# Optimization experiments

Hardware: AMD Instinct MI355X
Metric: run time of the kernel (lower is better)

## Reference

```python
import jax, jax.numpy as jnp
import numpy as np

B, NC, F, V, D = 16384, 13, 26, 100000, 16
H1, H2 = 400, 400
DNN_IN = NC + F * D  # 13 + 416 = 429


def setup_inputs() -> dict:
    key = jax.random.key(0)
    ks = jax.random.split(key, 12)
    s = 0.02
    return {
        "continuous": jax.random.normal(ks[0], (B, NC), jnp.float32),
        "cat_idx": jax.random.randint(ks[1], (B, F), 0, V),
        "W_cont": jax.random.normal(ks[2], (NC, 1), jnp.float32) * s,
        "b_cont": jnp.zeros((1,), jnp.float32),
        "emb_first": jax.random.normal(ks[3], (F, V), jnp.float32) * s,
        "emb": jax.random.normal(ks[4], (F, V, D), jnp.float32) * s,
        "W1": jax.random.normal(ks[5], (DNN_IN, H1), jnp.float32) * s,
        "b1": jnp.zeros((H1,), jnp.float32),
        "W2": jax.random.normal(ks[6], (H1, H2), jnp.float32) * s,
        "b2": jnp.zeros((H2,), jnp.float32),
        "W_out": jax.random.normal(ks[7], (H2 + 1, 1), jnp.float32) * s,
        "b_out": jnp.zeros((1,), jnp.float32),
    }


def reference(continuous, cat_idx, W_cont, b_cont, emb_first, emb, W1, b1, W2, b2, W_out, b_out):
    f_ids = jnp.arange(F)  # column ids
    # FM first-order: continuous linear + per-column 1-dim embedding gather, summed over columns
    fm1_cat = emb_first[f_ids[None, :], cat_idx]          # [B, F]
    fm1 = continuous @ W_cont + b_cont + jnp.sum(fm1_cat, axis=1, keepdims=True)  # [B, 1]
    # FM second-order: per-column D-dim embedding gather
    E = emb[f_ids[None, :], cat_idx]                      # [B, F, D]
    sum_emb = jnp.sum(E, axis=1)                          # [B, D]
    fm2 = 0.5 * jnp.sum(sum_emb * sum_emb - jnp.sum(E * E, axis=1), axis=1, keepdims=True)  # [B, 1]
    fm_out = fm1 + fm2
    # DNN on [continuous | flattened embeddings]; Dropout(0.0) is identity
    dnn_in = jnp.concatenate([continuous, E.reshape(E.shape[0], -1)], axis=1)  # [B, 429]
    h = jax.nn.relu(dnn_in @ W1 + b1)
    h = jax.nn.relu(h @ W2 + b2)
    fusion = jnp.concatenate([fm_out, h], axis=1)         # [B, H2+1]
    return fusion @ W_out + b_out                          # [B, 1]
```

## Files before the change

kernel.cpp:

```cpp
#include <hip/hip_runtime.h>
#include <hip/hip_bf16.h>
#include <stdint.h>

#define NB    16384
#define NCONT 13
#define NF    26
#define NV    100000
#define ND    16
#define NH    400
#define K1    448
#define KP1   456
#define K2    416
#define KP2   424
#define ROWS  64

typedef __attribute__((ext_vector_type(8))) __bf16 bf16x8;
typedef __attribute__((ext_vector_type(8))) short short8;
typedef __attribute__((ext_vector_type(4))) float f32x4;

__device__ __forceinline__ short f2bf(float x) {
  union { float f; uint32_t u; } c; c.f = x;
  uint32_t r = (c.u + 0x7FFFu + ((c.u >> 16) & 1u)) >> 16;
  return (short)(uint16_t)r;
}

__global__ __launch_bounds__(256)
void prep_k(const float* __restrict__ W1, const float* __restrict__ W2,
            short* __restrict__ W1T, short* __restrict__ W2T) {
  int t = blockIdx.x * 256 + threadIdx.x;
  if (t < NH * K1) {
    int n = t / K1, k = t - n * K1;
    float v = 0.f;
    if (k < 416)       v = W1[(size_t)(13 + k) * NH + n];
    else if (k < 429)  v = W1[(size_t)(k - 416) * NH + n];
    W1T[t] = f2bf(v);
  } else {
    int u = t - NH * K1;
    int n = u / K2, k = u - n * K2;
    float v = (k < NH) ? W2[(size_t)k * NH + n] : 0.f;
    W2T[u] = f2bf(v);
  }
}

template <int K, int KP>
__device__ __forceinline__ void layer(const short* __restrict__ WT, const short* lds,
                                      int wave, bool w0, int lrow, int kq,
                                      f32x4 acc[4][7]) {
  const short* wb = WT + (size_t)(wave * 16 + lrow) * K + kq;
  bf16x8 wf[2][7], af[2][4];
#pragma unroll
  for (int j = 0; j < 7; j++)
    if (j < 6 || w0) wf[0][j] = *(const bf16x8*)(wb + (size_t)j * 64 * K);
#pragma unroll
  for (int i = 0; i < 4; i++)
    af[0][i] = *(const bf16x8*)(lds + (i * 16 + lrow) * KP + kq);
#pragma unroll
  for (int ks = 0; ks < K / 32; ks++) {
    const int cur = ks & 1, nxt = cur ^ 1;
    if (ks + 1 < K / 32) {
#pragma unroll
      for (int j = 0; j < 7; j++)
        if (j < 6 || w0)
          wf[nxt][j] = *(const bf16x8*)(wb + (size_t)j * 64 * K + (ks + 1) * 32);
#pragma unroll
      for (int i = 0; i < 4; i++)
        af[nxt][i] = *(const bf16x8*)(lds + (i * 16 + lrow) * KP + (ks + 1) * 32 + kq);
    }
#pragma unroll
    for (int i = 0; i < 4; i++)
#pragma unroll
      for (int j = 0; j < 7; j++)
        if (j < 6 || w0)
          acc[i][j] = __builtin_amdgcn_mfma_f32_16x16x32_bf16(af[cur][i], wf[cur][j], acc[i][j], 0, 0, 0);
  }
}

__global__ __launch_bounds__(256, 1)
void fused_k(const float* __restrict__ cont, const int* __restrict__ cat,
             const float* __restrict__ Wc, const float* __restrict__ bc,
             const float* __restrict__ emb1, const float* __restrict__ emb,
             const short* __restrict__ W1T, const float* __restrict__ b1,
             const short* __restrict__ W2T, const float* __restrict__ b2,
             const float* __restrict__ Wout, const float* __restrict__ bout,
             float* __restrict__ out) {
  __shared__ short buf[ROWS * KP1];
  __shared__ float lP[4][ROWS];
  __shared__ float lFM[ROWS];
  short* lA = buf;
  short* lH = buf;
  const int tid = threadIdx.x;
  const int bm = blockIdx.x * ROWS;

  {
    const int q  = tid & 3;
    const int rl = tid >> 2;
    const int b  = bm + rl;
    float se[16];
#pragma unroll
    for (int d = 0; d < 16; d++) se[d] = 0.f;
    float sumsq = 0.f, fm1 = 0.f;
    short* drow = lA + rl * KP1;

#pragma unroll
    for (int fi = 0; fi < 7; fi++) {
      const int f = q + 4 * fi;
      if (f < NF) {
        int idx = cat[(size_t)b * NF + f];
        const float4* ep = (const float4*)(emb + ((size_t)f * NV + idx) * ND);
        float4 e0 = ep[0], e1 = ep[1], e2 = ep[2], e3 = ep[3];
        fm1 += emb1[(size_t)f * NV + idx];
        se[0] += e0.x; se[1] += e0.y; se[2] += e0.z; se[3] += e0.w;
        se[4] += e1.x; se[5] += e1.y; se[6] += e1.z; se[7] += e1.w;
        se[8] += e2.x; se[9] += e2.y; se[10] += e2.z; se[11] += e2.w;
        se[12] += e3.x; se[13] += e3.y; se[14] += e3.z; se[15] += e3.w;
        sumsq += e0.x*e0.x + e0.y*e0.y + e0.z*e0.z + e0.w*e0.w
               + e1.x*e1.x + e1.y*e1.y + e1.z*e1.z + e1.w*e1.w
               + e2.x*e2.x + e2.y*e2.y + e2.z*e2.z + e2.w*e2.w
               + e3.x*e3.x + e3.y*e3.y + e3.z*e3.z + e3.w*e3.w;
        short8 p0, p1;
        p0[0]=f2bf(e0.x); p0[1]=f2bf(e0.y); p0[2]=f2bf(e0.z); p0[3]=f2bf(e0.w);
        p0[4]=f2bf(e1.x); p0[5]=f2bf(e1.y); p0[6]=f2bf(e1.z); p0[7]=f2bf(e1.w);
        p1[0]=f2bf(e2.x); p1[1]=f2bf(e2.y); p1[2]=f2bf(e2.z); p1[3]=f2bf(e2.w);
        p1[4]=f2bf(e3.x); p1[5]=f2bf(e3.y); p1[6]=f2bf(e3.z); p1[7]=f2bf(e3.w);
        *(short8*)(drow + f * 16)     = p0;
        *(short8*)(drow + f * 16 + 8) = p1;
      }
    }
#pragma unroll
    for (int d = 0; d < 16; d++) {
      se[d] += __shfl_xor(se[d], 1, 64);
      se[d] += __shfl_xor(se[d], 2, 64);
    }
    sumsq += __shfl_xor(sumsq, 1, 64);
    sumsq += __shfl_xor(sumsq, 2, 64);
    fm1   += __shfl_xor(fm1, 1, 64);
    fm1   += __shfl_xor(fm1, 2, 64);

    if (q == 0) {
      float s2 = 0.f;
#pragma unroll
      for (int d = 0; d < 16; d++) s2 += se[d] * se[d];
      float fm2 = 0.5f * (s2 - sumsq);
      float fmc = bc[0];
      short tail[32];
#pragma unroll
      for (int i = 0; i < NCONT; i++) {
        float c = cont[(size_t)b * NCONT + i];
        fmc += c * Wc[i];
        tail[i] = f2bf(c);
      }
#pragma unroll
      for (int i = NCONT; i < 32; i++) tail[i] = 0;
#pragma unroll
      for (int v = 0; v < 4; v++) {
        short8 tv;
#pragma unroll
        for (int e = 0; e < 8; e++) tv[e] = tail[v * 8 + e];
        *(short8*)(drow + 416 + v * 8) = tv;
      }
      lFM[rl] = fm1 + fmc + fm2;
    }
  }
  __syncthreads();

  const int lane = tid & 63;
  const int wave = tid >> 6;
  const int lrow = lane & 15;
  const int quad = lane >> 4;
  const int kq   = quad * 8;
  const bool w0  = (wave == 0);
  f32x4 acc[4][7];

#pragma unroll
  for (int i = 0; i < 4; i++)
#pragma unroll
    for (int j = 0; j < 7; j++)
#pragma unroll
      for (int r = 0; r < 4; r++) acc[i][j][r] = 0.f;
  layer<K1, KP1>(W1T, lA, wave, w0, lrow, kq, acc);

  __syncthreads();

#pragma unroll
  for (int j = 0; j < 7; j++) {
    if (j < 6 || w0) {
      int col = (wave + 4 * j) * 16 + lrow;
      float bias = b1[col];
#pragma unroll
      for (int i = 0; i < 4; i++)
#pragma unroll
        for (int r = 0; r < 4; r++) {
          int row = i * 16 + quad * 4 + r;
          lH[row * KP2 + col] = f2bf(fmaxf(acc[i][j][r] + bias, 0.f));
        }
    }
  }
  {
    int row = tid >> 2, g = tid & 3;
    *(uint2*)&lH[row * KP2 + 400 + g * 4] = make_uint2(0u, 0u);
  }
  __syncthreads();

#pragma unroll
  for (int i = 0; i < 4; i++)
#pragma unroll
    for (int j = 0; j < 7; j++)
#pragma unroll
      for (int r = 0; r < 4; r++) acc[i][j][r] = 0.f;
  layer<K2, KP2>(W2T, lH, wave, w0, lrow, kq, acc);

  {
    float bw[7], wo[7];
#pragma unroll
    for (int j = 0; j < 7; j++) {
      bw[j] = 0.f; wo[j] = 0.f;
      if (j < 6 || w0) {
        int col = (wave + 4 * j) * 16 + lrow;
        bw[j] = b2[col];
        wo[j] = Wout[1 + col];
      }
    }
#pragma unroll
    for (int i = 0; i < 4; i++) {
#pragma unroll
      for (int r = 0; r < 4; r++) {
        float s = 0.f;
#pragma unroll
        for (int j = 0; j < 7; j++)
          if (j < 6 || w0) s += fmaxf(acc[i][j][r] + bw[j], 0.f) * wo[j];
        s += __shfl_xor(s, 1, 64);
        s += __shfl_xor(s, 2, 64);
        s += __shfl_xor(s, 4, 64);
        s += __shfl_xor(s, 8, 64);
        if (lrow == 0) lP[wave][i * 16 + quad * 4 + r] = s;
      }
    }
  }
  __syncthreads();

  if (tid < ROWS)
    out[bm + tid] = lFM[tid] * Wout[0] + bout[0]
                  + lP[0][tid] + lP[1][tid] + lP[2][tid] + lP[3][tid];
}

extern "C" void kernel_launch(void* const* d_in, const int* in_sizes, int n_in,
                              void* d_out, int out_size, void* d_ws, size_t ws_size,
                              hipStream_t stream) {
  const float* cont   = (const float*)d_in[0];
  const int*   cat    = (const int*)d_in[1];
  const float* W_cont = (const float*)d_in[2];
  const float* b_cont = (const float*)d_in[3];
  const float* emb1   = (const float*)d_in[4];
  const float* emb    = (const float*)d_in[5];
  const float* W1     = (const float*)d_in[6];
  const float* b1     = (const float*)d_in[7];
  const float* W2     = (const float*)d_in[8];
  const float* b2     = (const float*)d_in[9];
  const float* W_out  = (const float*)d_in[10];
  const float* b_out  = (const float*)d_in[11];
  float* out = (float*)d_out;

  char* ws = (char*)d_ws;
  short* W1T = (short*)ws;
  short* W2T = (short*)(ws + (size_t)NH * K1 * 2);
  (void)ws_size; (void)in_sizes; (void)n_in; (void)out_size;

  prep_k<<<dim3((NH * K1 + NH * K2 + 255) / 256), dim3(256), 0, stream>>>(W1, W2, W1T, W2T);
  fused_k<<<dim3(NB / ROWS), dim3(256), 0, stream>>>(cont, cat, W_cont, b_cont,
                                                     emb1, emb, W1T, b1, W2T, b2,
                                                     W_out, b_out, out);
}
```

Before: 271.0 us.

## Fuse weight transpose prep into main kernel with grid-wide flag barrier

```diff
diff --git a/kernel.cpp b/kernel.cpp
--- a/kernel.cpp
+++ b/kernel.cpp
@@ -13,6 +13,10 @@
 #define K2    416
 #define KP2   424
 #define ROWS  64
+#define NW1   (NH * K1)
+#define NTOT  (NH * K1 + NH * K2)
+#define PREPB ((NTOT + 255) / 256)
+#define MAGIC 0x5EED0001u
 
 typedef __attribute__((ext_vector_type(8))) __bf16 bf16x8;
 typedef __attribute__((ext_vector_type(8))) short short8;
@@ -22,24 +26,6 @@
   union { float f; uint32_t u; } c; c.f = x;
   uint32_t r = (c.u + 0x7FFFu + ((c.u >> 16) & 1u)) >> 16;
   return (short)(uint16_t)r;
-}
-
-__global__ __launch_bounds__(256)
-void prep_k(const float* __restrict__ W1, const float* __restrict__ W2,
-            short* __restrict__ W1T, short* __restrict__ W2T) {
-  int t = blockIdx.x * 256 + threadIdx.x;
-  if (t < NH * K1) {
-    int n = t / K1, k = t - n * K1;
-    float v = 0.f;
-    if (k < 416)       v = W1[(size_t)(13 + k) * NH + n];
-    else if (k < 429)  v = W1[(size_t)(k - 416) * NH + n];
-    W1T[t] = f2bf(v);
-  } else {
-    int u = t - NH * K1;
-    int n = u / K2, k = u - n * K2;
-    float v = (k < NH) ? W2[(size_t)k * NH + n] : 0.f;
-    W2T[u] = f2bf(v);
-  }
 }
 
 template <int K, int KP>
@@ -79,9 +65,11 @@
 void fused_k(const float* __restrict__ cont, const int* __restrict__ cat,
              const float* __restrict__ Wc, const float* __restrict__ bc,
              const float* __restrict__ emb1, const float* __restrict__ emb,
-             const short* __restrict__ W1T, const float* __restrict__ b1,
-             const short* __restrict__ W2T, const float* __restrict__ b2,
+             const float* __restrict__ W1, const float* __restrict__ b1,
+             const float* __restrict__ W2, const float* __restrict__ b2,
              const float* __restrict__ Wout, const float* __restrict__ bout,
+             short* __restrict__ W1T, short* __restrict__ W2T,
+             uint32_t* __restrict__ flags,
              float* __restrict__ out) {
   __shared__ short buf[ROWS * KP1];
   __shared__ float lP[4][ROWS];
@@ -90,6 +78,35 @@
   short* lH = buf;
   const int tid = threadIdx.x;
   const int bm = blockIdx.x * ROWS;
+
+  {
+    const int base = blockIdx.x * PREPB;
+#pragma unroll
+    for (int i = 0; i < (PREPB + 255) / 256; i++) {
+      int o = i * 256 + tid;
+      if (o < PREPB) {
+        int g = base + o;
+        if (g < NW1) {
+          int n = g / K1, k = g - n * K1;
+          float v = 0.f;
+          if (k < 416)       v = W1[(size_t)(13 + k) * NH + n];
+          else if (k < 429)  v = W1[(size_t)(k - 416) * NH + n];
+          W1T[g] = f2bf(v);
+        } else if (g < NTOT) {
+          int u = g - NW1;
+          int n = u / K2, k = u - n * K2;
+          float v = (k < NH) ? W2[(size_t)k * NH + n] : 0.f;
+          W2T[u] = f2bf(v);
+        }
+      }
+    }
+  }
+  __syncthreads();
+  if (tid == 0) {
+    __threadfence();
+    __hip_atomic_store(&flags[blockIdx.x], MAGIC,
+                       __ATOMIC_RELEASE, __HIP_MEMORY_SCOPE_AGENT);
+  }
 
   {
     const int q  = tid & 3;
@@ -161,6 +178,18 @@
       lFM[rl] = fm1 + fmc + fm2;
     }
   }
+
+  if (tid < 64) {
+    for (;;) {
+      uint32_t v0 = __hip_atomic_load(&flags[tid],       __ATOMIC_ACQUIRE, __HIP_MEMORY_SCOPE_AGENT);
+      uint32_t v1 = __hip_atomic_load(&flags[tid + 64],  __ATOMIC_ACQUIRE, __HIP_MEMORY_SCOPE_AGENT);
+      uint32_t v2 = __hip_atomic_load(&flags[tid + 128], __ATOMIC_ACQUIRE, __HIP_MEMORY_SCOPE_AGENT);
+      uint32_t v3 = __hip_atomic_load(&flags[tid + 192], __ATOMIC_ACQUIRE, __HIP_MEMORY_SCOPE_AGENT);
+      bool done = (v0 == MAGIC) && (v1 == MAGIC) && (v2 == MAGIC) && (v3 == MAGIC);
+      if (__all(done)) break;
+      __builtin_amdgcn_s_sleep(2);
+    }
+  }
   __syncthreads();
 
   const int lane = tid & 63;
@@ -261,12 +290,12 @@
   float* out = (float*)d_out;
 
   char* ws = (char*)d_ws;
-  short* W1T = (short*)ws;
-  short* W2T = (short*)(ws + (size_t)NH * K1 * 2);
+  short*    W1T   = (short*)ws;
+  short*    W2T   = (short*)(ws + (size_t)NH * K1 * 2);
+  uint32_t* flags = (uint32_t*)(ws + (size_t)NH * (K1 + K2) * 2);
   (void)ws_size; (void)in_sizes; (void)n_in; (void)out_size;
 
-  prep_k<<<dim3((NH * K1 + NH * K2 + 255) / 256), dim3(256), 0, stream>>>(W1, W2, W1T, W2T);
   fused_k<<<dim3(NB / ROWS), dim3(256), 0, stream>>>(cont, cat, W_cont, b_cont,
-                                                     emb1, emb, W1T, b1, W2T, b2,
-                                                     W_out, b_out, out);
+                                                     emb1, emb, W1, b1, W2, b2,
+                                                     W_out, b_out, W1T, W2T, flags, out);
 }
```

After: 295.3 us. +8.9%, slower.
